# Optimization experiments

Hardware: AMD Instinct MI355X
Metric: run time of the kernel (lower is better)

## Reference

```python
import jax, jax.numpy as jnp
import numpy as np

W_BIJ, W_ORTH, W_LAP, W_PRE = 1000.0, 1000.0, 1.0, 100000.0
N, V, C, K = 8, 5000, 128, 128
NUM_DESC = int(C * 0.2)  # 25, matches sub_pre=0.2


def setup_inputs() -> dict:
    key = jax.random.key(0)
    ks = jax.random.split(key, 10)
    return {
        "C12": jax.random.normal(ks[0], (N, K, K), jnp.float32) * 0.1,
        "C21": jax.random.normal(ks[1], (N, K, K), jnp.float32) * 0.1,
        "feat_1": jax.random.normal(ks[2], (N, V, C), jnp.float32),
        "feat_2": jax.random.normal(ks[3], (N, V, C), jnp.float32),
        "evecs_1": jax.random.normal(ks[4], (N, V, K), jnp.float32) * 0.02,
        "evecs_2": jax.random.normal(ks[5], (N, V, K), jnp.float32) * 0.02,
        "evecs_trans1": jax.random.normal(ks[6], (N, K, V), jnp.float32) * 0.02,
        "evecs_trans2": jax.random.normal(ks[7], (N, K, V), jnp.float32) * 0.02,
        "evals_1": jax.random.uniform(ks[8], (N, K), jnp.float32),
        "evals_2": jax.random.uniform(ks[9], (N, K), jnp.float32),
        "desc_ind": jnp.arange(NUM_DESC, dtype=jnp.int32),
    }


def _frob3(a, b):
    # torch FrobeniusLoss on [N,K,K]: mean over batch of sum((a-b)^2, dims (1,2))
    return jnp.mean(jnp.sum((a - b) ** 2, axis=(1, 2)))


def reference(C12, C21, feat_1, feat_2, evecs_1, evecs_2,
              evecs_trans1, evecs_trans2, evals_1, evals_2, desc_ind):
    n, k, _ = C12.shape
    eye = jnp.eye(k, dtype=C12.dtype)[None]  # broadcasts over batch

    l_bij = (_frob3(jnp.einsum('nij,njk->nik', C12, C21), eye)
             + _frob3(jnp.einsum('nij,njk->nik', C21, C12), eye)) * W_BIJ

    l_orth = (_frob3(jnp.einsum('nji,njk->nik', C12, C12), eye)
              + _frob3(jnp.einsum('nji,njk->nik', C21, C21), eye)) * W_ORTH

    # diag-scale commutativity: C * evals (col scale) vs evals * C (row scale)
    l_lap = (_frob3(C12 * evals_1[:, None, :], evals_2[:, :, None] * C12)
             + _frob3(C21 * evals_2[:, None, :], evals_1[:, :, None] * C21)) * W_LAP

    # descriptor preservation via commutativity, D = num_desc subsampled channels
    f1 = feat_1[:, :, desc_ind]  # [N,V,D]
    f2 = feat_2[:, :, desc_ind]
    # M[n,d] = Phi_trans @ diag(f[:,d]) @ Phi  (KxK per descriptor), fused einsum
    M1 = jnp.einsum('nkv,nvd,nvj->ndkj', evecs_trans1, f1, evecs_1)
    M2 = jnp.einsum('nkv,nvd,nvj->ndkj', evecs_trans2, f2, evecs_2)
    s1 = jnp.einsum('nij,ndjk->ndik', C12, M1)  # C12 @ M1_d
    t1 = jnp.einsum('ndij,njk->ndik', M2, C12)  # M2_d @ C12
    s2 = jnp.einsum('nij,ndjk->ndik', C21, M2)
    t2 = jnp.einsum('ndij,njk->ndik', M1, C21)
    # torch FrobeniusLoss on 5D [N,D,1,K,K]: sum over axes (1,2), then global mean
    # over remaining [N,K,K] -> total_sum / (N*K*K)
    denom = jnp.asarray(n * k * k, s1.dtype)
    l_pre = ((jnp.sum((s1 - t1) ** 2) + jnp.sum((s2 - t2) ** 2)) / denom) * W_PRE

    return jnp.stack([l_bij, l_orth, l_lap, l_pre])
```

## Files before the change

kernel.cpp:

```cpp
#include <hip/hip_runtime.h>

typedef float v4f __attribute__((ext_vector_type(4)));
typedef unsigned int u32;
typedef __attribute__((ext_vector_type(2))) u32 u32x2;
typedef __attribute__((ext_vector_type(4))) u32 u32x4;
typedef __attribute__((ext_vector_type(8))) short bhalf8;

#define K 128
#define W_BIJ 1000.0f
#define W_ORTH 1000.0f
#define W_LAP 1.0f
#define W_PRE 100000.0f

#define NCH 79
#define TILE_B 16384
#define CTILE_B 32768
#define VPAD 5120

union B8 { u32x4 u; bhalf8 h; };

static __device__ __forceinline__ unsigned short f2b(float x) {
    union { float f; unsigned int u; } v; v.f = x;
    unsigned int u = v.u + 0x7FFFu + ((v.u >> 16) & 1u);
    return (unsigned short)(u >> 16);
}
static __device__ __forceinline__ u32 pk2(float lo, float hi) {
    return (u32)f2b(lo) | ((u32)f2b(hi) << 16);
}
static __device__ __forceinline__ float bitsf(u32 x) {
    union { u32 u; float f; } v; v.u = x; return v.f;
}
static __device__ __forceinline__ u32 cvtpk(float lo, float hi) {
    u32 r; asm("v_cvt_pk_bf16_f32 %0, %1, %2" : "=v"(r) : "v"(lo), "v"(hi)); return r;
}
static __device__ __forceinline__ void gload_lds16(const void* g, void* l) {
    __builtin_amdgcn_global_load_lds((const __attribute__((address_space(1))) u32*)g,
                                     (__attribute__((address_space(3))) u32*)l, 16, 0, 0);
}

extern "C" __global__ __launch_bounds__(256, 2)
void surfm_conv(const float* __restrict__ T1, const float* __restrict__ T2,
                const float* __restrict__ E1, const float* __restrict__ E2,
                const float* __restrict__ F1, const float* __restrict__ F2,
                const float* __restrict__ C12g, const float* __restrict__ C21g,
                const int* __restrict__ desc,
                unsigned short* __restrict__ Abf, unsigned short* __restrict__ Ebf,
                float* __restrict__ Fbf, char* __restrict__ Cbf,
                int V, int CF)
{
    __shared__ char csm[36992];
    const int b = blockIdx.x;
    const int tid = threadIdx.x;

    if (b < 1264) {
        const int c  = b % NCH;
        const int mn = b / NCH;
        const float* src = ((mn & 8) ? T2 : T1) + (size_t)(mn & 7) * K * V;
        char* dst = (char*)Abf + (size_t)b * TILE_B;
        #pragma unroll
        for (int it = 0; it < 4; ++it) {
            const int item = it * 256 + tid;
            const int grp = item & 7, r = item >> 3;
            const int kg = grp ^ (r & 7);
            const int k = c * 64 + kg * 8;
            u32x4 o = (u32x4){0u,0u,0u,0u};
            if (k + 8 <= V) {
                const v4f lo = *(const v4f*)(src + (size_t)r * V + k);
                const v4f hi = *(const v4f*)(src + (size_t)r * V + k + 4);
                o[0] = pk2(lo[0], lo[1]); o[1] = pk2(lo[2], lo[3]);
                o[2] = pk2(hi[0], hi[1]); o[3] = pk2(hi[2], hi[3]);
            }
            *(u32x4*)(dst + r * 128 + grp * 16) = o;
        }
    } else if (b < 2528) {
        const int idx = b - 1264;
        const int c  = idx % NCH;
        const int mn = idx / NCH;
        const float* src = ((mn & 8) ? E2 : E1) + (size_t)(mn & 7) * V * K;
        char* dst = (char*)Ebf + (size_t)idx * TILE_B;
        #pragma unroll
        for (int it = 0; it < 8; ++it) {
            const int item = it * 256 + tid;
            const int vp = item >> 5;
            const int j4 = (item & 31) * 4;
            const int v = c * 64 + vp * 2;
            v4f e0 = {0.f,0.f,0.f,0.f}, e1 = e0;
            if (v < V)     e0 = *(const v4f*)(src + (size_t)v * K + j4);
            if (v + 1 < V) e1 = *(const v4f*)(src + (size_t)(v + 1) * K + j4);
            #pragma unroll
            for (int e = 0; e < 4; ++e) {
                const int j = j4 + e;
                *(u32*)(csm + j * 128 + vp * 4) = pk2(e0[e], e1[e]);
            }
        }
        __syncthreads();
        #pragma unroll
        for (int it = 0; it < 4; ++it) {
            const int item = it * 256 + tid;
            *(u32x4*)(dst + item * 16) = *(const u32x4*)(csm + item * 16);
        }
    } else if (b < 2688) {
        const int idx = b - 2528;
        const int vc = idx % 10;
        const int mn = idx / 10;
        const float* src = ((mn & 8) ? F2 : F1) + (size_t)(mn & 7) * V * CF;
        float* dstB = Fbf + (size_t)(mn * 25) * VPAD + vc * 512;
        int* sdesc = (int*)csm;
        float* stg = (float*)(csm + 128);
        if (tid < 25) sdesc[tid] = desc[tid];
        #pragma unroll 1
        for (int pass = 0; pass < 8; ++pass) {
            const int vbase = vc * 512 + pass * 64;
            __syncthreads();
            #pragma unroll
            for (int it = 0; it < 8; ++it) {
                const int item = it * 256 + tid;
                const int vloc = item >> 5;
                const int c4 = (item & 31) * 4;
                const int v = vbase + vloc;
                v4f x = {0.f,0.f,0.f,0.f};
                if (v < V) x = *(const v4f*)(src + (size_t)v * CF + c4);
                float* p = stg + vloc * 129 + c4;
                p[0] = x[0]; p[1] = x[1]; p[2] = x[2]; p[3] = x[3];
            }
            __syncthreads();
            for (int i = tid; i < 1600; i += 256) {
                const int d = i >> 6, vloc = i & 63;
                dstB[(size_t)d * VPAD + pass * 64 + vloc] = stg[vloc * 129 + sdesc[d]];
            }
        }
    } else {
        const int idx = b - 2688;
        const float* src = ((idx & 8) ? C21g : C12g) + (size_t)(idx & 7) * K * K;
        char* outN = Cbf + (size_t)(idx * 2 + 0) * CTILE_B;
        char* outT = Cbf + (size_t)(idx * 2 + 1) * CTILE_B;
        #pragma unroll
        for (int it = 0; it < 8; ++it) {
            const int item = it * 256 + tid;
            const int r = item >> 4, grp = item & 15;
            const int g = grp ^ (r & 7);
            const v4f lo = *(const v4f*)(src + r * K + g * 8);
            const v4f hi = *(const v4f*)(src + r * K + g * 8 + 4);
            u32x4 o;
            o[0] = pk2(lo[0], lo[1]); o[1] = pk2(lo[2], lo[3]);
            o[2] = pk2(hi[0], hi[1]); o[3] = pk2(hi[2], hi[3]);
            *(u32x4*)(outN + r * 256 + grp * 16) = o;
        }
        #pragma unroll
        for (int it = 0; it < 8; ++it) {
            const int item = it * 256 + tid;
            const int rp = item >> 5;
            const int j4 = (item & 31) * 4;
            const v4f r0 = *(const v4f*)(src + (2 * rp) * K + j4);
            const v4f r1 = *(const v4f*)(src + (2 * rp + 1) * K + j4);
            #pragma unroll
            for (int e = 0; e < 4; ++e) {
                const int j = j4 + e;
                *(u32*)(csm + j * 256 + ((rp * 4) ^ ((j & 7) << 4))) = pk2(r0[e], r1[e]);
            }
        }
        __syncthreads();
        #pragma unroll
        for (int it = 0; it < 8; ++it) {
            const int item = it * 256 + tid;
            *(u32x4*)(outT + item * 16) = *(const u32x4*)(csm + item * 16);
        }
    }
}

extern "C" __global__ __launch_bounds__(512, 4)
void surfm_stage1(const char* __restrict__ Abf, const char* __restrict__ Ebf,
                  const float* __restrict__ Fbf, char* __restrict__ MpartB)
{
    extern __shared__ char sm[];
    const int tid = threadIdx.x;
    const int l  = tid & 63;
    const int wq = __builtin_amdgcn_readfirstlane(tid >> 6);
    const int b = blockIdx.x;
    const int n = b & 7;
    const int rest = b >> 3;
    const int mat = rest & 1;
    const int vq  = (rest >> 1) & 3;
    const int dgi = rest >> 3;
    const int d0 = dgi * 2;
    const bool hasD1 = (d0 + 1) < 25;

    const int mn = mat * 8 + n;
    const char* gA = Abf + (size_t)mn * NCH * TILE_B;
    const char* gE = Ebf + (size_t)mn * NCH * TILE_B;
    const char* gW = (const char*)(Fbf + ((size_t)mn * 25 + d0) * VPAD) + vq * 5120;
    const int c0 = vq * 20;
    const int NT = (vq == 3) ? 19 : 20;

    const int lm = l & 15;
    const int lk = (l >> 4) * 8;
    const int j  = wq * 16 + lm;
    const int rkey = (lm & 7) << 4;
    float* wLds = (float*)(sm + 32768);

    v4f acc0[8], acc1[8];
    #pragma unroll
    for (int mf = 0; mf < 8; ++mf) {
        acc0[mf] = (v4f){0.f,0.f,0.f,0.f};
        acc1[mf] = (v4f){0.f,0.f,0.f,0.f};
    }

    for (int i = wq; i < 10; i += 8)
        gload_lds16(gW + (i / 5) * (VPAD * 4) + (i % 5) * 1024 + l * 16,
                    sm + 32768 + (i / 5) * 5120 + (i % 5) * 1024);
    {
        const char* t = gA + (size_t)c0 * TILE_B;
        gload_lds16(t + (wq * 2 + 0) * 1024 + l * 16, sm + (wq * 2 + 0) * 1024);
        gload_lds16(t + (wq * 2 + 1) * 1024 + l * 16, sm + (wq * 2 + 1) * 1024);
    }
    const char* gEl = gE + j * 128 + lk * 2;
    u32x4 eC0 = *(const u32x4*)(gEl + (size_t)c0 * TILE_B);
    u32x4 eC1 = *(const u32x4*)(gEl + (size_t)c0 * TILE_B + 64);
    asm volatile("s_waitcnt vmcnt(0)" ::: "memory");
    __builtin_amdgcn_s_barrier();

    #pragma unroll 1
    for (int t = 0; t < NT; ++t) {
        const int par = t & 1;
        u32x4 eN0 = eC0, eN1 = eC1;
        if (t + 1 < NT) {
            const char* tA = gA + (size_t)(c0 + t + 1) * TILE_B;
            char* dA = sm + (par ^ 1) * 16384;
            gload_lds16(tA + (wq * 2 + 0) * 1024 + l * 16, dA + (wq * 2 + 0) * 1024);
            gload_lds16(tA + (wq * 2 + 1) * 1024 + l * 16, dA + (wq * 2 + 1) * 1024);
            const char* tE = gEl + (size_t)(c0 + t + 1) * TILE_B;
            eN0 = *(const u32x4*)(tE);
            eN1 = *(const u32x4*)(tE + 64);
        }

        const char* Ab = sm + par * 16384;
        #pragma unroll
        for (int ks = 0; ks < 2; ++ks) {
            const u32x4 e = ks ? eC1 : eC0;
            const float* pw0 = wLds + t * 64 + ks * 32 + lk;
            const float* pw1 = pw0 + 1280;
            const v4f w0a = *(const v4f*)pw0, w0b = *(const v4f*)(pw0 + 4);
            const v4f w1a = *(const v4f*)pw1, w1b = *(const v4f*)(pw1 + 4);
            const float wl0[4] = {w0a[0], w0a[2], w0b[0], w0b[2]};
            const float wh0[4] = {w0a[1], w0a[3], w0b[1], w0b[3]};
            const float wl1[4] = {w1a[0], w1a[2], w1b[0], w1b[2]};
            const float wh1[4] = {w1a[1], w1a[3], w1b[1], w1b[3]};
            B8 p0, p1;
            #pragma unroll
            for (int t4 = 0; t4 < 4; ++t4) {
                const float elo = bitsf(e[t4] << 16);
                const float ehi = bitsf(e[t4] & 0xFFFF0000u);
                p0.u[t4] = cvtpk(elo * wl0[t4], ehi * wh0[t4]);
                if (hasD1) p1.u[t4] = cvtpk(elo * wl1[t4], ehi * wh1[t4]);
            }
            const int kb = ks * 64 + lk * 2;
            #pragma unroll
            for (int mf = 0; mf < 8; ++mf) {
                const int r = mf * 16 + lm;
                B8 a; a.u = *(const u32x4*)(Ab + r * 128 + (kb ^ rkey));
                acc0[mf] = __builtin_amdgcn_mfma_f32_16x16x32_bf16(a.h, p0.h, acc0[mf], 0, 0, 0);
                if (hasD1)
                    acc1[mf] = __builtin_amdgcn_mfma_f32_16x16x32_bf16(a.h, p1.h, acc1[mf], 0, 0, 0);
            }
        }
        eC0 = eN0; eC1 = eN1;

        if (t + 1 < NT) {
            asm volatile("s_waitcnt vmcnt(0)" ::: "memory");
            __builtin_amdgcn_s_barrier();
        }
    }

    const int slotM = (n * 25 + d0) * 2 + mat;
    const int rbyte = (l >> 4) * 8;
    {
        char* dst = MpartB + ((size_t)(vq * 400 + slotM)) * 32768 + j * 256 + rbyte;
        #pragma unroll
        for (int mf = 0; mf < 8; ++mf) {
            u32x2 o;
            o[0] = pk2(acc0[mf][0], acc0[mf][1]);
            o[1] = pk2(acc0[mf][2], acc0[mf][3]);
            *(u32x2*)(dst + mf * 32) = o;
        }
    }
    if (hasD1) {
        char* dst = MpartB + ((size_t)(vq * 400 + slotM + 2)) * 32768 + j * 256 + rbyte;
        #pragma unroll
        for (int mf = 0; mf < 8; ++mf) {
            u32x2 o;
            o[0] = pk2(acc1[mf][0], acc1[mf][1]);
            o[1] = pk2(acc1[mf][2], acc1[mf][3]);
            *(u32x2*)(dst + mf * 32) = o;
        }
    }
}

extern "C" __global__ __launch_bounds__(256, 2)
void surfm_mconv(const char* __restrict__ MpartB, char* __restrict__ Mbf)
{
    extern __shared__ char sm[];
    float* sMT = (float*)sm;
    const int s = blockIdx.x;
    const int tid = threadIdx.x;
    const char* p0 = MpartB + (size_t)s * 32768;
    for (int i = tid; i < 2048; i += 256) {
        const int jj = i >> 4, g = i & 15;
        float sum[8] = {0.f,0.f,0.f,0.f,0.f,0.f,0.f,0.f};
        #pragma unroll
        for (int p = 0; p < 4; ++p) {
            const u32x4 v = *(const u32x4*)(p0 + (size_t)p * 400 * 32768 + jj * 256 + g * 16);
            #pragma unroll
            for (int e = 0; e < 4; ++e) {
                sum[2 * e + 0] += bitsf(v[e] << 16);
                sum[2 * e + 1] += bitsf(v[e] & 0xFFFF0000u);
            }
        }
        float* q = sMT + jj * 132 + g * 8;
        #pragma unroll
        for (int e = 0; e < 8; ++e) q[e] = sum[e];
    }
    __syncthreads();
    char* outN = Mbf + (size_t)s * 65536;
    char* outT = outN + 32768;
    #pragma unroll
    for (int it = 0; it < 16; ++it) {
        const int item = it * 256 + tid;
        const int lay = item >> 11;
        const int g2 = item & 2047;
        const int rr = g2 >> 4, grp = g2 & 15;
        const int g = grp ^ (rr & 7);
        u32x4 o;
        if (lay == 0) {
            const float* p = sMT + rr * 132 + g * 8;
            const v4f a = *(const v4f*)p, bq = *(const v4f*)(p + 4);
            o[0] = pk2(a[0], a[1]);   o[1] = pk2(a[2], a[3]);
            o[2] = pk2(bq[0], bq[1]); o[3] = pk2(bq[2], bq[3]);
            *(u32x4*)(outT + rr * 256 + grp * 16) = o;
        } else {
            const float* p = sMT + (g * 8) * 132 + rr;
            o[0] = pk2(p[0],   p[132]); o[1] = pk2(p[264], p[396]);
            o[2] = pk2(p[528], p[660]); o[3] = pk2(p[792], p[924]);
            *(u32x4*)(outN + rr * 256 + grp * 16) = o;
        }
    }
}

extern "C" __global__ __launch_bounds__(256, 1)
void surfm_stage2(const float* __restrict__ C12g, const float* __restrict__ C21g,
                  const float* __restrict__ ev1g, const float* __restrict__ ev2g,
                  const char* __restrict__ Cbf, const char* __restrict__ Mbf,
                  float* __restrict__ out, int N, int ND)
{
    extern __shared__ char sm[];
    const int b = blockIdx.x;
    const int tid = threadIdx.x;
    const int nPre = N * ND;

    if (b < nPre) {
        const int n = b & 7, d = b >> 3;
        const size_t slot = n * 25 + d;
        const int l = tid & 63;
        const int wq = __builtin_amdgcn_readfirstlane(tid >> 6);
        const int lm = l & 15, lk = (l >> 4) * 8;
        const int wm = wq >> 1, wj = wq & 1;
        float rsum = 0.0f;

        #pragma unroll 1
        for (int ph = 0; ph < 2; ++ph) {
            const char* s0 = Cbf + ((size_t)(ph * 8 + n) * 2 + 0) * CTILE_B;
            const char* s1 = Mbf + (slot * 2 + (ph ? 1 : 0)) * 65536 + 32768;
            const char* s2 = Mbf + (slot * 2 + (ph ? 0 : 1)) * 65536;
            const char* s3 = Cbf + ((size_t)(ph * 8 + n) * 2 + 1) * CTILE_B;
            const char* gs = (wq == 0) ? s0 : (wq == 1) ? s1 : (wq == 2) ? s2 : s3;
            char* ld = sm + wq * 32768;
            if (ph) __builtin_amdgcn_s_barrier();
            #pragma unroll
            for (int i = 0; i < 32; ++i)
                gload_lds16(gs + i * 1024 + l * 16, ld + i * 1024);
            asm volatile("s_waitcnt vmcnt(0)" ::: "memory");
            __builtin_amdgcn_s_barrier();
            __builtin_amdgcn_sched_barrier(0);

            v4f as_[4][4], at_[4][4];
            #pragma unroll
            for (int mf = 0; mf < 4; ++mf)
                #pragma unroll
                for (int jf = 0; jf < 4; ++jf) {
                    as_[mf][jf] = (v4f){0.f,0.f,0.f,0.f};
                    at_[mf][jf] = (v4f){0.f,0.f,0.f,0.f};
                }
            #pragma unroll
            for (int ks = 0; ks < 4; ++ks) {
                const int kb = ks * 64 + lk * 2;
                B8 bS[4], bT[4];
                #pragma unroll
                for (int jf = 0; jf < 4; ++jf) {
                    const int jj = wj * 64 + jf * 16 + lm;
                    const int off = jj * 256 + (kb ^ ((jj & 7) << 4));
                    bS[jf].u = *(const u32x4*)(sm + 32768 + off);
                    bT[jf].u = *(const u32x4*)(sm + 98304 + off);
                }
                #pragma unroll
                for (int mf = 0; mf < 4; ++mf) {
                    const int r = wm * 64 + mf * 16 + lm;
                    const int off = r * 256 + (kb ^ ((r & 7) << 4));
                    B8 aS; aS.u = *(const u32x4*)(sm + off);
                    B8 aT; aT.u = *(const u32x4*)(sm + 65536 + off);
                    #pragma unroll
                    for (int jf = 0; jf < 4; ++jf) {
                        as_[mf][jf] = __builtin_amdgcn_mfma_f32_16x16x32_bf16(aS.h, bS[jf].h, as_[mf][jf], 0, 0, 0);
                        at_[mf][jf] = __builtin_amdgcn_mfma_f32_16x16x32_bf16(aT.h, bT[jf].h, at_[mf][jf], 0, 0, 0);
                    }
                }
            }
            #pragma unroll
            for (int mf = 0; mf < 4; ++mf)
                #pragma unroll
                for (int jf = 0; jf < 4; ++jf) {
                    const v4f df = as_[mf][jf] - at_[mf][jf];
                    rsum += df[0]*df[0] + df[1]*df[1] + df[2]*df[2] + df[3]*df[3];
                }
        }
        #pragma unroll
        for (int off = 32; off; off >>= 1) rsum += __shfl_down(rsum, off, 64);
        if (l == 0)
            atomicAdd(out + 3, rsum * (W_PRE / (float)(N * K * K)));
    } else {
        float* lds = (float*)sm;
        const int idx = b - nPre;
        const int n = idx >> 2, p = idx & 3;
        const float* c12 = C12g + (size_t)n * K * K;
        const float* c21 = C21g + (size_t)n * K * K;
        const float* Xg = (p == 1 || p == 3) ? c21 : c12;
        const float* Yg = (p == 0) ? c21 : c12;
        const float* ea = (p == 0) ? ev1g + n * K : ev2g + n * K;
        const float* eb = (p == 0) ? ev2g + n * K : ev1g + n * K;
        float* X = lds;
        float* Y = lds + K * 129;
        const int tx = tid & 15, ty = tid >> 4;
        float lap = 0.0f;
        for (int i = tid; i < K * K / 4; i += 256) {
            const int r = i >> 5, c4 = (i & 31) * 4;
            const v4f x = *(const v4f*)(Xg + r * K + c4);
            X[r * 129 + c4 + 0] = x[0]; X[r * 129 + c4 + 1] = x[1];
            X[r * 129 + c4 + 2] = x[2]; X[r * 129 + c4 + 3] = x[3];
            if (p < 2) {
                const v4f y = *(const v4f*)(Yg + r * K + c4);
                Y[r * 129 + c4 + 0] = y[0]; Y[r * 129 + c4 + 1] = y[1];
                Y[r * 129 + c4 + 2] = y[2]; Y[r * 129 + c4 + 3] = y[3];
                const float ebi = eb[r];
                #pragma unroll
                for (int e = 0; e < 4; ++e) {
                    const float dlt = ea[c4 + e] - ebi;
                    lap += x[e] * x[e] * dlt * dlt;
                }
            }
        }
        __syncthreads();
        const int i0 = ty * 8, k0 = tx * 8;
        float z[8][8];
        #pragma unroll
        for (int i = 0; i < 8; ++i)
            #pragma unroll
            for (int t = 0; t < 8; ++t) z[i][t] = 0.0f;
        for (int jj = 0; jj < K; ++jj) {
            float xi[8], yk[8];
            if (p < 2) {
                #pragma unroll
                for (int i = 0; i < 8; ++i) xi[i] = X[(i0 + i) * 129 + jj];
                #pragma unroll
                for (int t = 0; t < 8; ++t) yk[t] = Y[jj * 129 + k0 + t];
            } else {
                #pragma unroll
                for (int i = 0; i < 8; ++i) xi[i] = X[jj * 129 + i0 + i];
                #pragma unroll
                for (int t = 0; t < 8; ++t) yk[t] = X[jj * 129 + k0 + t];
            }
            #pragma unroll
            for (int i = 0; i < 8; ++i)
                #pragma unroll
                for (int t = 0; t < 8; ++t) z[i][t] += xi[i] * yk[t];
        }
        float sacc = 0.0f;
        #pragma unroll
        for (int i = 0; i < 8; ++i)
            #pragma unroll
            for (int t = 0; t < 8; ++t) {
                const float e = z[i][t] - ((i0 + i) == (k0 + t) ? 1.0f : 0.0f);
                sacc += e * e;
            }
        #pragma unroll
        for (int off = 32; off; off >>= 1) {
            sacc += __shfl_down(sacc, off, 64);
            lap  += __shfl_down(lap, off, 64);
        }
        if ((tid & 63) == 0) {
            if (p < 2) {
                atomicAdd(out + 0, sacc * (W_BIJ / (float)N));
                atomicAdd(out + 2, lap * (W_LAP / (float)N));
            } else {
                atomicAdd(out + 1, sacc * (W_ORTH / (float)N));
            }
        }
    }
}

extern "C" __global__ __launch_bounds__(256, 1)
void surfm_fused(const float* __restrict__ C12g, const float* __restrict__ C21g,
                 const float* __restrict__ F1, const float* __restrict__ F2,
                 const float* __restrict__ E1g, const float* __restrict__ E2g,
                 const float* __restrict__ T1, const float* __restrict__ T2,
                 const float* __restrict__ ev1g, const float* __restrict__ ev2g,
                 const int* __restrict__ desc, float* __restrict__ out,
                 int N, int ND, int V, int CF)
{
    extern __shared__ char smem[];
    const int b   = blockIdx.x;
    const int tid = threadIdx.x;
    const int nPre = N * ND;

    if (b < nPre) {
        const int n = b & 7;
        const int d = b >> 3;
        const int col = desc[d];
        const float* A1g = T1 + (size_t)n * K * V;
        const float* A2g = T2 + (size_t)n * K * V;
        const float* B1g = E1g + (size_t)n * V * K;
        const float* B2g = E2g + (size_t)n * V * K;
        const float* w1g = F1 + (size_t)n * V * CF;
        const float* w2g = F2 + (size_t)n * V * CF;

        char* As1 = smem;
        char* As2 = smem + 32768;
        char* Bt1 = smem + 65536;
        char* Bt2 = smem + 98304;

        const int l  = tid & 63;
        const int w  = tid >> 6;
        const int lm = l & 15;
        const int lk = (l >> 4) * 8;

        v4f acc1[8][2], acc2[8][2];
        #pragma unroll
        for (int mf = 0; mf < 8; ++mf)
            #pragma unroll
            for (int jf = 0; jf < 2; ++jf) {
                acc1[mf][jf] = (v4f){0.f,0.f,0.f,0.f};
                acc2[mf][jf] = (v4f){0.f,0.f,0.f,0.f};
            }

        for (int v0 = 0; v0 < V; v0 += 128) {
            __syncthreads();
            #pragma unroll 4
            for (int it = 0; it < 16; ++it) {
                const int i  = it * 256 + tid;
                const int r  = i >> 5;
                const int c4 = (i & 31) * 4;
                const int vg = v0 + c4;
                v4f a1 = {0.f,0.f,0.f,0.f}, a2 = {0.f,0.f,0.f,0.f};
                if (vg < V) {
                    a1 = *(const v4f*)(A1g + (size_t)r * V + vg);
                    a2 = *(const v4f*)(A2g + (size_t)r * V + vg);
                }
                const int byte = (r * 256 + c4 * 2) ^ ((r & 7) << 4);
                short4 p1, p2;
                p1.x = (short)f2b(a1[0]); p1.y = (short)f2b(a1[1]);
                p1.z = (short)f2b(a1[2]); p1.w = (short)f2b(a1[3]);
                p2.x = (short)f2b(a2[0]); p2.y = (short)f2b(a2[1]);
                p2.z = (short)f2b(a2[2]); p2.w = (short)f2b(a2[3]);
                *(short4*)(As1 + byte) = p1;
                *(short4*)(As2 + byte) = p2;
            }
            #pragma unroll 2
            for (int it = 0; it < 8; ++it) {
                const int i  = it * 256 + tid;
                const int j4 = (i & 31) * 4;
                const int vp = (i >> 5) * 2;
                const int va = v0 + vp, vb = va + 1;
                v4f e1a = {0.f,0.f,0.f,0.f}, e1b = e1a, e2a = e1a, e2b = e1a;
                if (va < V) {
                    const float w1 = w1g[(size_t)va * CF + col];
                    const float w2 = w2g[(size_t)va * CF + col];
                    e1a = *(const v4f*)(B1g + (size_t)va * K + j4) * w1;
                    e2a = *(const v4f*)(B2g + (size_t)va * K + j4) * w2;
                }
                if (vb < V) {
                    const float w1 = w1g[(size_t)vb * CF + col];
                    const float w2 = w2g[(size_t)vb * CF + col];
                    e1b = *(const v4f*)(B1g + (size_t)vb * K + j4) * w1;
                    e2b = *(const v4f*)(B2g + (size_t)vb * K + j4) * w2;
                }
                #pragma unroll
                for (int e = 0; e < 4; ++e) {
                    const int j = j4 + e;
                    const int key = (((j & 7) ^ ((j >> 3) & 7)) << 4);
                    const int byte = (j * 256 + vp * 2) ^ key;
                    *(u32*)(Bt1 + byte) = pk2(e1a[e], e1b[e]);
                    *(u32*)(Bt2 + byte) = pk2(e2a[e], e2b[e]);
                }
            }
            __syncthreads();
            #pragma unroll
            for (int ks = 0; ks < 4; ++ks) {
                const int k0 = ks * 32 + lk;
                bhalf8 bB1[2], bB2[2];
                #pragma unroll
                for (int jf = 0; jf < 2; ++jf) {
                    const int j = w * 32 + jf * 16 + lm;
                    const int key = (((j & 7) ^ ((j >> 3) & 7)) << 4);
                    const int byte = (j * 256 + k0 * 2) ^ key;
                    bB1[jf] = *(const bhalf8*)(Bt1 + byte);
                    bB2[jf] = *(const bhalf8*)(Bt2 + byte);
                }
                #pragma unroll
                for (int mf = 0; mf < 8; ++mf) {
                    const int r = mf * 16 + lm;
                    const int byte = (r * 256 + k0 * 2) ^ ((r & 7) << 4);
                    const bhalf8 a1 = *(const bhalf8*)(As1 + byte);
                    const bhalf8 a2 = *(const bhalf8*)(As2 + byte);
                    acc1[mf][0] = __builtin_amdgcn_mfma_f32_16x16x32_bf16(a1, bB1[0], acc1[mf][0], 0, 0, 0);
                    acc1[mf][1] = __builtin_amdgcn_mfma_f32_16x16x32_bf16(a1, bB1[1], acc1[mf][1], 0, 0, 0);
                    acc2[mf][0] = __builtin_amdgcn_mfma_f32_16x16x32_bf16(a2, bB2[0], acc2[mf][0], 0, 0, 0);
                    acc2[mf][1] = __builtin_amdgcn_mfma_f32_16x16x32_bf16(a2, bB2[1], acc2[mf][1], 0, 0, 0);
                }
            }
        }
        __syncthreads();
        float* M1 = (float*)smem;
        float* M2 = (float*)smem + K * K;
        #pragma unroll
        for (int mf = 0; mf < 8; ++mf)
            #pragma unroll
            for (int jf = 0; jf < 2; ++jf)
                #pragma unroll
                for (int rg = 0; rg < 4; ++rg) {
                    const int row = mf * 16 + ((l >> 4) << 2) + rg;
                    const int cj  = w * 32 + jf * 16 + lm;
                    const int pc  = ((((cj >> 2) ^ ((row >> 3) & 7)) << 2) | (cj & 3));
                    M1[row * K + pc] = acc1[mf][jf][rg];
                    M2[row * K + pc] = acc2[mf][jf][rg];
                }
        __syncthreads();

        const int tx = tid & 15, ty = tid >> 4;
        const int r0 = ty * 8;
        const int ca = tx * 4, cb = 64 + tx * 4;
        const int kcol = ty & 7;
        const float* c12 = C12g + (size_t)n * K * K;
        const float* c21 = C21g + (size_t)n * K * K;
        v4f acc1a[8], acc1b[8], acc2a[8], acc2b[8];
        #pragma unroll
        for (int i = 0; i < 8; ++i) {
            acc1a[i] = (v4f){0,0,0,0}; acc1b[i] = (v4f){0,0,0,0};
            acc2a[i] = (v4f){0,0,0,0}; acc2b[i] = (v4f){0,0,0,0};
        }
        for (int jj = 0; jj < K; ++jj) {
            const int keyj = (jj >> 3) & 7;
            const int ga = (tx ^ keyj) << 2;
            const int gb = ((16 + tx) ^ keyj) << 2;
            const v4f m1ra = *(const v4f*)(M1 + jj * K + ga);
            const v4f m1rb = *(const v4f*)(M1 + jj * K + gb);
            const v4f m2ra = *(const v4f*)(M2 + jj * K + ga);
            const v4f m2rb = *(const v4f*)(M2 + jj * K + gb);
            const v4f c12ra = *(const v4f*)(c12 + jj * K + ca);
            const v4f c12rb = *(const v4f*)(c12 + jj * K + cb);
            const v4f c21ra = *(const v4f*)(c21 + jj * K + ca);
            const v4f c21rb = *(const v4f*)(c21 + jj * K + cb);
            const int jp = (((jj >> 2) ^ kcol) << 2) | (jj & 3);
            #pragma unroll
            for (int i = 0; i < 8; ++i) {
                const int r = r0 + i;
                const float x12 = c12[r * K + jj];
                const float x21 = c21[r * K + jj];
                const float m1c = M1[r * K + jp];
                const float m2c = M2[r * K + jp];
                acc1a[i] += m1ra * x12; acc1a[i] -= c12ra * m2c;
                acc1b[i] += m1rb * x12; acc1b[i] -= c12rb * m2c;
                acc2a[i] += m2ra * x21; acc2a[i] -= c21ra * m1c;
                acc2b[i] += m2rb * x21; acc2b[i] -= c21rb * m1c;
            }
        }
        float s = 0.0f;
        #pragma unroll
        for (int i = 0; i < 8; ++i)
            #pragma unroll
            for (int e = 0; e < 4; ++e) {
                s += acc1a[i][e] * acc1a[i][e] + acc1b[i][e] * acc1b[i][e];
                s += acc2a[i][e] * acc2a[i][e] + acc2b[i][e] * acc2b[i][e];
            }
        #pragma unroll
        for (int off = 32; off; off >>= 1) s += __shfl_down(s, off, 64);
        if ((tid & 63) == 0)
            atomicAdd(out + 3, s * (W_PRE / (float)(N * K * K)));
    } else {
        float* ldsf = (float*)smem;
        const int idx = b - nPre;
        const int n = idx >> 2, p = idx & 3;
        const float* c12 = C12g + (size_t)n * K * K;
        const float* c21 = C21g + (size_t)n * K * K;
        const float* Xg = (p == 1 || p == 3) ? c21 : c12;
        const float* Yg = (p == 0) ? c21 : c12;
        const float* ea = (p == 0) ? ev1g + n * K : ev2g + n * K;
        const float* eb = (p == 0) ? ev2g + n * K : ev1g + n * K;
        float* X = ldsf;
        float* Y = ldsf + K * 129;
        const int tx = tid & 15, ty = tid >> 4;
        float lap = 0.0f;
        for (int i = tid; i < K * K / 4; i += 256) {
            const int r = i >> 5, c4 = (i & 31) * 4;
            const v4f x = *(const v4f*)(Xg + r * K + c4);
            X[r * 129 + c4 + 0] = x[0]; X[r * 129 + c4 + 1] = x[1];
            X[r * 129 + c4 + 2] = x[2]; X[r * 129 + c4 + 3] = x[3];
            if (p < 2) {
                const v4f y = *(const v4f*)(Yg + r * K + c4);
                Y[r * 129 + c4 + 0] = y[0]; Y[r * 129 + c4 + 1] = y[1];
                Y[r * 129 + c4 + 2] = y[2]; Y[r * 129 + c4 + 3] = y[3];
                const float ebi = eb[r];
                #pragma unroll
                for (int e = 0; e < 4; ++e) {
                    const float dlt = ea[c4 + e] - ebi;
                    lap += x[e] * x[e] * dlt * dlt;
                }
            }
        }
        __syncthreads();
        const int i0 = ty * 8, k0 = tx * 8;
        float z[8][8];
        #pragma unroll
        for (int i = 0; i < 8; ++i)
            #pragma unroll
            for (int t = 0; t < 8; ++t) z[i][t] = 0.0f;
        for (int jj = 0; jj < K; ++jj) {
            float xi[8], yk[8];
            if (p < 2) {
                #pragma unroll
                for (int i = 0; i < 8; ++i) xi[i] = X[(i0 + i) * 129 + jj];
                #pragma unroll
                for (int t = 0; t < 8; ++t) yk[t] = Y[jj * 129 + k0 + t];
            } else {
                #pragma unroll
                for (int i = 0; i < 8; ++i) xi[i] = X[jj * 129 + i0 + i];
                #pragma unroll
                for (int t = 0; t < 8; ++t) yk[t] = X[jj * 129 + k0 + t];
            }
            #pragma unroll
            for (int i = 0; i < 8; ++i)
                #pragma unroll
                for (int t = 0; t < 8; ++t) z[i][t] += xi[i] * yk[t];
        }
        float s = 0.0f;
        #pragma unroll
        for (int i = 0; i < 8; ++i)
            #pragma unroll
            for (int t = 0; t < 8; ++t) {
                const float e = z[i][t] - ((i0 + i) == (k0 + t) ? 1.0f : 0.0f);
                s += e * e;
            }
        #pragma unroll
        for (int off = 32; off; off >>= 1) {
            s   += __shfl_down(s, off, 64);
            lap += __shfl_down(lap, off, 64);
        }
        if ((tid & 63) == 0) {
            if (p < 2) {
                atomicAdd(out + 0, s * (W_BIJ / (float)N));
                atomicAdd(out + 2, lap * (W_LAP / (float)N));
            } else {
                atomicAdd(out + 1, s * (W_ORTH / (float)N));
            }
        }
    }
}

extern "C" void kernel_launch(void* const* d_in, const int* in_sizes, int n_in,
                              void* d_out, int out_size, void* d_ws, size_t ws_size,
                              hipStream_t stream) {
    (void)n_in;
    const float* C12 = (const float*)d_in[0];
    const float* C21 = (const float*)d_in[1];
    const float* F1  = (const float*)d_in[2];
    const float* F2  = (const float*)d_in[3];
    const float* E1  = (const float*)d_in[4];
    const float* E2  = (const float*)d_in[5];
    const float* T1  = (const float*)d_in[6];
    const float* T2  = (const float*)d_in[7];
    const float* ev1 = (const float*)d_in[8];
    const float* ev2 = (const float*)d_in[9];
    const int* desc  = (const int*)d_in[10];
    float* out = (float*)d_out;

    const int N  = in_sizes[8] / K;
    const int ND = in_sizes[10];
    const int V  = in_sizes[4] / (N * K);
    const int CF = in_sizes[2] / (N * V);

    hipMemsetAsync(d_out, 0, (size_t)out_size * sizeof(float), stream);

    const size_t ABF = (size_t)16 * NCH * TILE_B;
    const size_t EBF = ABF;
    const size_t FBF = (size_t)400 * VPAD * 4;
    const size_t CBF = (size_t)32 * CTILE_B;
    const size_t MBF = (size_t)400 * 65536;
    const size_t MPB = (size_t)4 * 400 * 32768;
    const size_t base = ABF + EBF + FBF + CBF + MBF;
    const size_t needPart = base + MPB;

    const bool okShape = (N == 8 && ND == 25 && V == 5000 && CF == 128);
    if (!okShape || ws_size < needPart) {
        const size_t shmem = (size_t)(2 * K * 129) * sizeof(float);
        hipFuncSetAttribute((const void*)surfm_fused,
                            hipFuncAttributeMaxDynamicSharedMemorySize, (int)shmem);
        const int blocks = N * ND + 4 * N;
        surfm_fused<<<blocks, 256, shmem, stream>>>(C12, C21, F1, F2, E1, E2, T1, T2,
                                                    ev1, ev2, desc, out, N, ND, V, CF);
        return;
    }

    char* ws = (char*)d_ws;
    unsigned short* Abf = (unsigned short*)ws;
    unsigned short* Ebf = (unsigned short*)(ws + ABF);
    float* Fbf = (float*)(ws + ABF + EBF);
    char* Cbf = ws + ABF + EBF + FBF;
    char* Mbf = ws + ABF + EBF + FBF + CBF;
    char* MpartB = ws + base;

    surfm_conv<<<2704, 256, 0, stream>>>(T1, T2, E1, E2, F1, F2, C12, C21, desc,
                                         Abf, Ebf, Fbf, Cbf, V, CF);

    const size_t shmem1 = 43008;
    hipFuncSetAttribute((const void*)surfm_stage1,
                        hipFuncAttributeMaxDynamicSharedMemorySize, (int)shmem1);
    surfm_stage1<<<832, 512, shmem1, stream>>>((const char*)Abf, (const char*)Ebf,
                                               Fbf, MpartB);

    const size_t shmemM = (size_t)128 * 132 * 4;
    hipFuncSetAttribute((const void*)surfm_mconv,
                        hipFuncAttributeMaxDynamicSharedMemorySize, (int)shmemM);
    surfm_mconv<<<400, 256, shmemM, stream>>>(MpartB, Mbf);

    const size_t shmem2 = 132096;
    hipFuncSetAttribute((const void*)surfm_stage2,
                        hipFuncAttributeMaxDynamicSharedMemorySize, (int)shmem2);
    surfm_stage2<<<N * ND + 4 * N, 256, shmem2, stream>>>(C12, C21, ev1, ev2,
                                                          Cbf, Mbf, out, N, ND);
}
```

Baseline: 197.1 us.

## Triple-buffer stage1 A tiles and gather descriptor columns with per-descriptor blocks

Stage1 moves from double to triple buffering of the A tile in LDS. It prefetches two tiles ahead and waits with vmcnt(2) so global loads overlap more of the MFMA work, and raises s_setprio around the MFMA loop. The feature-descriptor gather in the conversion kernel now uses one block per (matrix, descriptor), reading the selected column with strided scalar loads instead of staging through LDS. This adds 16KB of LDS per stage1 block, which may lower occupancy, and the strided column reads are uncoalesced.

```diff
diff --git a/kernel.cpp b/kernel.cpp
--- a/kernel.cpp
+++ b/kernel.cpp
@@ -99,38 +99,17 @@
             const int item = it * 256 + tid;
             *(u32x4*)(dst + item * 16) = *(const u32x4*)(csm + item * 16);
         }
-    } else if (b < 2688) {
+    } else if (b < 2928) {
         const int idx = b - 2528;
-        const int vc = idx % 10;
-        const int mn = idx / 10;
-        const float* src = ((mn & 8) ? F2 : F1) + (size_t)(mn & 7) * V * CF;
-        float* dstB = Fbf + (size_t)(mn * 25) * VPAD + vc * 512;
-        int* sdesc = (int*)csm;
-        float* stg = (float*)(csm + 128);
-        if (tid < 25) sdesc[tid] = desc[tid];
-        #pragma unroll 1
-        for (int pass = 0; pass < 8; ++pass) {
-            const int vbase = vc * 512 + pass * 64;
-            __syncthreads();
-            #pragma unroll
-            for (int it = 0; it < 8; ++it) {
-                const int item = it * 256 + tid;
-                const int vloc = item >> 5;
-                const int c4 = (item & 31) * 4;
-                const int v = vbase + vloc;
-                v4f x = {0.f,0.f,0.f,0.f};
-                if (v < V) x = *(const v4f*)(src + (size_t)v * CF + c4);
-                float* p = stg + vloc * 129 + c4;
-                p[0] = x[0]; p[1] = x[1]; p[2] = x[2]; p[3] = x[3];
-            }
-            __syncthreads();
-            for (int i = tid; i < 1600; i += 256) {
-                const int d = i >> 6, vloc = i & 63;
-                dstB[(size_t)d * VPAD + pass * 64 + vloc] = stg[vloc * 129 + sdesc[d]];
-            }
-        }
+        const int d  = idx % 25;
+        const int mn = idx / 25;
+        const int col = desc[d];
+        const float* src = ((mn & 8) ? F2 : F1) + (size_t)(mn & 7) * V * CF + col;
+        float* dst = Fbf + (size_t)idx * VPAD;
+        for (int i = tid; i < VPAD; i += 256)
+            dst[i] = (i < V) ? src[(size_t)i * CF] : 0.0f;
     } else {
-        const int idx = b - 2688;
+        const int idx = b - 2928;
         const float* src = ((idx & 8) ? C21g : C12g) + (size_t)(idx & 7) * K * K;
         char* outN = Cbf + (size_t)(idx * 2 + 0) * CTILE_B;
         char* outT = Cbf + (size_t)(idx * 2 + 1) * CTILE_B;
@@ -196,7 +175,7 @@
     const int lk = (l >> 4) * 8;
     const int j  = wq * 16 + lm;
     const int rkey = (lm & 7) << 4;
-    float* wLds = (float*)(sm + 32768);
+    float* wLds = (float*)(sm + 49152);
 
     v4f acc0[8], acc1[8];
     #pragma unroll
@@ -205,35 +184,44 @@
         acc1[mf] = (v4f){0.f,0.f,0.f,0.f};
     }
 
+    const char* gEl = gE + j * 128 + lk * 2;
+
     for (int i = wq; i < 10; i += 8)
         gload_lds16(gW + (i / 5) * (VPAD * 4) + (i % 5) * 1024 + l * 16,
-                    sm + 32768 + (i / 5) * 5120 + (i % 5) * 1024);
+                    sm + 49152 + (i / 5) * 5120 + (i % 5) * 1024);
     {
-        const char* t = gA + (size_t)c0 * TILE_B;
-        gload_lds16(t + (wq * 2 + 0) * 1024 + l * 16, sm + (wq * 2 + 0) * 1024);
-        gload_lds16(t + (wq * 2 + 1) * 1024 + l * 16, sm + (wq * 2 + 1) * 1024);
-    }
-    const char* gEl = gE + j * 128 + lk * 2;
+        const char* tA = gA + (size_t)c0 * TILE_B;
+        gload_lds16(tA + (wq * 2 + 0) * 1024 + l * 16, sm + (wq * 2 + 0) * 1024);
+        gload_lds16(tA + (wq * 2 + 1) * 1024 + l * 16, sm + (wq * 2 + 1) * 1024);
+    }
     u32x4 eC0 = *(const u32x4*)(gEl + (size_t)c0 * TILE_B);
     u32x4 eC1 = *(const u32x4*)(gEl + (size_t)c0 * TILE_B + 64);
-    asm volatile("s_waitcnt vmcnt(0)" ::: "memory");
+    {
+        const char* tA = gA + (size_t)(c0 + 1) * TILE_B;
+        gload_lds16(tA + (wq * 2 + 0) * 1024 + l * 16, sm + 16384 + (wq * 2 + 0) * 1024);
+        gload_lds16(tA + (wq * 2 + 1) * 1024 + l * 16, sm + 16384 + (wq * 2 + 1) * 1024);
+    }
+    asm volatile("s_waitcnt vmcnt(2)" ::: "memory");
     __builtin_amdgcn_s_barrier();
 
     #pragma unroll 1
     for (int t = 0; t < NT; ++t) {
-        const int par = t & 1;
+        const int bufC = t % 3;
         u32x4 eN0 = eC0, eN1 = eC1;
         if (t + 1 < NT) {
-            const char* tA = gA + (size_t)(c0 + t + 1) * TILE_B;
-            char* dA = sm + (par ^ 1) * 16384;
-            gload_lds16(tA + (wq * 2 + 0) * 1024 + l * 16, dA + (wq * 2 + 0) * 1024);
-            gload_lds16(tA + (wq * 2 + 1) * 1024 + l * 16, dA + (wq * 2 + 1) * 1024);
             const char* tE = gEl + (size_t)(c0 + t + 1) * TILE_B;
             eN0 = *(const u32x4*)(tE);
             eN1 = *(const u32x4*)(tE + 64);
         }
-
-        const char* Ab = sm + par * 16384;
+        if (t + 2 < NT) {
+            const char* tA = gA + (size_t)(c0 + t + 2) * TILE_B;
+            char* dA = sm + ((t + 2) % 3) * 16384;
+            gload_lds16(tA + (wq * 2 + 0) * 1024 + l * 16, dA + (wq * 2 + 0) * 1024);
+            gload_lds16(tA + (wq * 2 + 1) * 1024 + l * 16, dA + (wq * 2 + 1) * 1024);
+        }
+        __builtin_amdgcn_sched_barrier(0);
+
+        const char* Ab = sm + bufC * 16384;
         #pragma unroll
         for (int ks = 0; ks < 2; ++ks) {
             const u32x4 e = ks ? eC1 : eC0;
@@ -254,6 +242,7 @@
                 if (hasD1) p1.u[t4] = cvtpk(elo * wl1[t4], ehi * wh1[t4]);
             }
             const int kb = ks * 64 + lk * 2;
+            __builtin_amdgcn_s_setprio(1);
             #pragma unroll
             for (int mf = 0; mf < 8; ++mf) {
                 const int r = mf * 16 + lm;
@@ -262,11 +251,13 @@
                 if (hasD1)
                     acc1[mf] = __builtin_amdgcn_mfma_f32_16x16x32_bf16(a.h, p1.h, acc1[mf], 0, 0, 0);
             }
+            __builtin_amdgcn_s_setprio(0);
         }
         eC0 = eN0; eC1 = eN1;
 
         if (t + 1 < NT) {
-            asm volatile("s_waitcnt vmcnt(0)" ::: "memory");
+            if (t + 2 < NT) asm volatile("s_waitcnt vmcnt(2)" ::: "memory");
+            else            asm volatile("s_waitcnt vmcnt(0)" ::: "memory");
             __builtin_amdgcn_s_barrier();
         }
     }
@@ -824,10 +815,10 @@
     char* Mbf = ws + ABF + EBF + FBF + CBF;
     char* MpartB = ws + base;
 
-    surfm_conv<<<2704, 256, 0, stream>>>(T1, T2, E1, E2, F1, F2, C12, C21, desc,
+    surfm_conv<<<2944, 256, 0, stream>>>(T1, T2, E1, E2, F1, F2, C12, C21, desc,
                                          Abf, Ebf, Fbf, Cbf, V, CF);
 
-    const size_t shmem1 = 43008;
+    const size_t shmem1 = 59392;
     hipFuncSetAttribute((const void*)surfm_stage1,
                         hipFuncAttributeMaxDynamicSharedMemorySize, (int)shmem1);
     surfm_stage1<<<832, 512, shmem1, stream>>>((const char*)Abf, (const char*)Ebf,
```

Result: faster. 189.6 us (-3.8%).
